# Kernel tuning notes

Measured on AMD Instinct MI355X. Metric: run time of the kernel, lower is better.

## Reference

```python
import jax, jax.numpy as jnp
import numpy as np

B = 16        # number of point clouds
NP = 4096     # points per cloud
RATIO = 0.25
RADIUS = 0.2
K = 64        # max_num_neighbors hardcoded in the torch module
S = int(NP * RATIO)  # sampled centers per cloud
C_IN = 64


def setup_inputs() -> dict:
    key = jax.random.key(0)
    ks = jax.random.split(key, 6)
    x = jax.random.normal(ks[0], (B * NP, C_IN), dtype=jnp.float32)
    pos = jax.random.uniform(ks[1], (B * NP, 3), dtype=jnp.float32)  # unit cube
    batch = jnp.repeat(jnp.arange(B, dtype=jnp.int64), NP)
    d0, d1, d2, d3 = C_IN + 3, 64, 64, 128  # local_nn dims
    W1 = jax.random.normal(ks[2], (d0, d1), dtype=jnp.float32) / np.sqrt(d0)
    W2 = jax.random.normal(ks[3], (d1, d2), dtype=jnp.float32) / np.sqrt(d1)
    W3 = jax.random.normal(ks[4], (d2, d3), dtype=jnp.float32) / np.sqrt(d2)
    b1 = jnp.zeros((d1,), jnp.float32)
    b2 = jnp.zeros((d2,), jnp.float32)
    b3 = jnp.zeros((d3,), jnp.float32)
    return {"x": x, "pos": pos, "batch": batch,
            "W1": W1, "b1": b1, "W2": W2, "b2": b2, "W3": W3, "b3": b3}


def _fps(pos_b):
    """Farthest point sampling for one cloud. pos_b: [NP,3] -> [S] int32 indices."""
    dmin = jnp.sum((pos_b - pos_b[0]) ** 2, axis=-1)  # start from point 0

    def step(dmin, _):
        idx = jnp.argmax(dmin).astype(jnp.int32)
        dmin = jnp.minimum(dmin, jnp.sum((pos_b - pos_b[idx]) ** 2, axis=-1))
        return dmin, idx

    _, idxs = jax.lax.scan(step, dmin, None, length=S - 1)
    return jnp.concatenate([jnp.zeros((1,), jnp.int32), idxs])


def reference(x, pos, batch, W1, b1, W2, b2, W3, b3):
    xb = x.reshape(B, NP, -1)
    pb = pos.reshape(B, NP, 3)

    def per_cloud(xb_, pb_):
        idxs = _fps(pb_)                      # [S]
        centers = pb_[idxs]                   # [S,3]
        # ball query: up to K nearest neighbors within RADIUS (center itself always in-range)
        d2 = jnp.sum((centers[:, None, :] - pb_[None, :, :]) ** 2, axis=-1)  # [S,NP]
        neg = jnp.where(d2 <= RADIUS * RADIUS, -d2, -jnp.inf)
        vals, nbr = jax.lax.top_k(neg, K)     # [S,K]
        valid = jnp.isfinite(vals)            # [S,K]
        # PointConv message: local_nn(concat(x_j, pos_j - pos_i)), max-aggregated
        xj = xb_[nbr]                         # [S,K,C]
        rel = pb_[nbr] - centers[:, None, :]  # [S,K,3]
        h = jnp.concatenate([xj, rel], axis=-1)
        h = jax.nn.relu(h @ W1 + b1)
        h = jax.nn.relu(h @ W2 + b2)
        h = h @ W3 + b3                       # [S,K,Cout]
        h = jnp.where(valid[..., None], h, -jnp.inf)
        return jnp.max(h, axis=1), centers    # [S,Cout], [S,3]

    out, centers = jax.vmap(per_cloud)(xb, pb)
    x_out = out.reshape(B * S, -1)
    pos_out = centers.reshape(B * S, 3)
    batch_out = jnp.repeat(jnp.arange(B, dtype=batch.dtype), S)
    return x_out, pos_out, batch_out
```

## Files before the change

kernel.cpp:

```cpp
#include <hip/hip_runtime.h>
#include <math.h>

#define NB   16
#define NPTS 4096
#define SS   1024
#define KK   64
#define CIN  64
#define TPB  512
#define NWORK 240
#define GRID (NB + NWORK)
#define WPREP_N 20480

typedef unsigned short ushort_t;
typedef float vf2 __attribute__((ext_vector_type(2)));
typedef unsigned long long vu2 __attribute__((ext_vector_type(2)));
typedef short bf8v __attribute__((ext_vector_type(8)));
typedef float f4v __attribute__((ext_vector_type(4)));

__device__ __forceinline__ float dist2(float ax, float ay, float az,
                                       float bx, float by, float bz) {
#pragma clang fp contract(off)
  float dx = ax - bx, dy = ay - by, dz = az - bz;
  float a = dx * dx, b = dy * dy, c = dz * dz;
  return (a + b) + c;
}

__device__ __forceinline__ vf2 dist2v(vf2 x, vf2 y, vf2 z,
                                      vf2 cx, vf2 cy, vf2 cz) {
#pragma clang fp contract(off)
  vf2 dx = x - cx, dy = y - cy, dz = z - cz;
  vf2 a = dx * dx, b = dy * dy, c = dz * dz;
  return (a + b) + c;
}

__device__ __forceinline__ ushort_t f2bf(float f) {
  unsigned u = __float_as_uint(f);
  return (ushort_t)((u + 0x7FFFu + ((u >> 16) & 1u)) >> 16);
}

#define DPPMAX(v, ctrl, rmask)                                                 \
  fmaxf((v), __int_as_float(__builtin_amdgcn_update_dpp(                       \
                 __float_as_int(v), __float_as_int(v), (ctrl), (rmask), 0xf,   \
                 false)))

__global__ __launch_bounds__(256) void wprep_kernel(
    const float* __restrict__ W1, const float* __restrict__ W2,
    const float* __restrict__ W3, ushort_t* __restrict__ wbuf) {
  int i = blockIdx.x * 256 + threadIdx.x;
  if (i >= WPREP_N) return;
  float v;
  if (i < 6656) {
    int n = i / 104, k = i - n * 104;
    v = (k < 67) ? W1[k * 64 + n] : 0.f;
  } else if (i < 11264) {
    int j = i - 6656;
    int n = j / 72, k = j - n * 72;
    v = (k < 64) ? W2[k * 64 + n] : 0.f;
  } else {
    int j = i - 11264;
    int n = j / 72, k = j - n * 72;
    v = (k < 64) ? W3[k * 128 + n] : 0.f;
  }
  wbuf[i] = f2bf(v);
}

struct FpsS {
  float px[NPTS], py[NPTS], pz[NPTS];
  unsigned long long swk[2][4];
};
struct WrkS {
  ushort_t feat[64][104];
  ushort_t h1[64][72];
  union {
    unsigned long long ckey[1024];
    ushort_t h2[64][72];
  } u;
  float red[4][128];
  int nbr_s[KK];
  float cctr[3];
  int scnt;
};

__global__ __launch_bounds__(TPB) void fused_kernel(
    const float* __restrict__ pos, const float* __restrict__ x,
    const ushort_t* __restrict__ wbuf,
    const float* __restrict__ b1, const float* __restrict__ b2,
    const float* __restrict__ b3,
    float* __restrict__ centers4, int* __restrict__ prog,
    float* __restrict__ out_x, float* __restrict__ out_pos,
    float* __restrict__ out_batch) {
  __shared__ __align__(16) union { FpsS f; WrkS w; } S;
  const int t = threadIdx.x;

  if (blockIdx.x < NB) {
    asm volatile("s_setprio 3");
    const int b = blockIdx.x;
    const float* p = pos + (size_t)b * NPTS * 3;

    for (int j = t; j < NPTS * 3; j += TPB) {
      float v = p[j];
      int pt = j / 3, ch = j - pt * 3;
      if (ch == 0) S.f.px[pt] = v;
      else if (ch == 1) S.f.py[pt] = v;
      else S.f.pz[pt] = v;
    }
    for (int j = t; j < SS; j += TPB) out_batch[b * SS + j] = (float)b;
    __syncthreads();

    if (t < 256) {
      const int base = t * 16;
      vf2 x2[8], y2[8], z2[8], dm2[8];
      const float c0x = S.f.px[0], c0y = S.f.py[0], c0z = S.f.pz[0];
      {
        vf2 cX = {c0x, c0x}, cY = {c0y, c0y}, cZ = {c0z, c0z};
#pragma unroll
        for (int u = 0; u < 8; ++u) {
          x2[u].x = S.f.px[base + 2 * u]; x2[u].y = S.f.px[base + 2 * u + 1];
          y2[u].x = S.f.py[base + 2 * u]; y2[u].y = S.f.py[base + 2 * u + 1];
          z2[u].x = S.f.pz[base + 2 * u]; z2[u].y = S.f.pz[base + 2 * u + 1];
          dm2[u] = dist2v(x2[u], y2[u], z2[u], cX, cY, cZ);
        }
      }
      const int lane = t & 63, wid = t >> 6;
      const float BIG = 1e9f;
      int parity = 0;
      for (int s = 1; s < SS; ++s) {
        vf2 m0 = __builtin_elementwise_max(dm2[0], dm2[1]);
        vf2 m1 = __builtin_elementwise_max(dm2[2], dm2[3]);
        vf2 m2 = __builtin_elementwise_max(dm2[4], dm2[5]);
        vf2 m3 = __builtin_elementwise_max(dm2[6], dm2[7]);
        vf2 mm = __builtin_elementwise_max(
            __builtin_elementwise_max(m0, m1), __builtin_elementwise_max(m2, m3));
        float bv = fmaxf(mm.x, mm.y);
        float wv = bv;
        wv = DPPMAX(wv, 0x111, 0xf);
        wv = DPPMAX(wv, 0x112, 0xf);
        wv = DPPMAX(wv, 0x114, 0xf);
        wv = DPPMAX(wv, 0x118, 0xf);
        wv = DPPMAX(wv, 0x142, 0xa);
        wv = DPPMAX(wv, 0x143, 0xc);
        const float gvw =
            __int_as_float(__builtin_amdgcn_readlane(__float_as_int(wv), 63));
        unsigned long long mk = __ballot(bv == gvw);
        int fl = __ffsll((long long)mk) - 1;
        vf2 fcnt = {0.f, 1.f};
        vf2 best = {BIG, BIG};
#pragma unroll
        for (int u = 0; u < 8; ++u) {
          vf2 sv;
          sv.x = (dm2[u].x == gvw) ? fcnt.x : BIG;
          sv.y = (dm2[u].y == gvw) ? fcnt.y : BIG;
          best = __builtin_elementwise_min(best, sv);
          fcnt += (vf2){2.f, 2.f};
        }
        const int li = (int)fminf(best.x, best.y);
        if (lane == fl) {
          int gi = base + li;
          S.f.swk[parity][wid] =
              ((unsigned long long)__float_as_uint(gvw) << 32) |
              (unsigned)(~(unsigned)gi);
        }
        __syncthreads();
        const vu2* sp = (const vu2*)(&S.f.swk[parity][0]);
        vu2 q0 = sp[0], q1 = sp[1];
        unsigned long long bk = q0.x;
        bk = (q0.y > bk) ? q0.y : bk;
        bk = (q1.x > bk) ? q1.x : bk;
        bk = (q1.y > bk) ? q1.y : bk;
        const int gi = (int)(~(unsigned)bk);
        const float cx = S.f.px[gi], cy = S.f.py[gi], cz = S.f.pz[gi];
        {
          vf2 cX = {cx, cx}, cY = {cy, cy}, cZ = {cz, cz};
#pragma unroll
          for (int u = 0; u < 8; ++u) {
            vf2 d2 = dist2v(x2[u], y2[u], z2[u], cX, cY, cZ);
            dm2[u] = __builtin_elementwise_min(dm2[u], d2);
          }
        }
        parity ^= 1;
      }
      return;
    } else if (t < 320) {
      if (t == 256) {
        int r = b * SS;
        float c0x = S.f.px[0], c0y = S.f.py[0], c0z = S.f.pz[0];
        __hip_atomic_store(&centers4[r * 4 + 0], c0x, __ATOMIC_RELAXED, __HIP_MEMORY_SCOPE_AGENT);
        __hip_atomic_store(&centers4[r * 4 + 1], c0y, __ATOMIC_RELAXED, __HIP_MEMORY_SCOPE_AGENT);
        __hip_atomic_store(&centers4[r * 4 + 2], c0z, __ATOMIC_RELAXED, __HIP_MEMORY_SCOPE_AGENT);
        out_pos[r * 3 + 0] = c0x; out_pos[r * 3 + 1] = c0y; out_pos[r * 3 + 2] = c0z;
      }
      int parity = 0;
      for (int s = 1; s < SS; ++s) {
        __syncthreads();
        if (t == 256) {
          if ((s & 1) == 0) {
            asm volatile("s_waitcnt vmcnt(6)" ::: "memory");
            __hip_atomic_store(&prog[b * 32], s - 1, __ATOMIC_RELAXED, __HIP_MEMORY_SCOPE_AGENT);
          }
          const vu2* sp = (const vu2*)(&S.f.swk[parity][0]);
          vu2 q0 = sp[0], q1 = sp[1];
          unsigned long long bk = q0.x;
          bk = (q0.y > bk) ? q0.y : bk;
          bk = (q1.x > bk) ? q1.x : bk;
          bk = (q1.y > bk) ? q1.y : bk;
          const int gi = (int)(~(unsigned)bk);
          const float cx = S.f.px[gi], cy = S.f.py[gi], cz = S.f.pz[gi];
          int r = b * SS + s;
          __hip_atomic_store(&centers4[r * 4 + 0], cx, __ATOMIC_RELAXED, __HIP_MEMORY_SCOPE_AGENT);
          __hip_atomic_store(&centers4[r * 4 + 1], cy, __ATOMIC_RELAXED, __HIP_MEMORY_SCOPE_AGENT);
          __hip_atomic_store(&centers4[r * 4 + 2], cz, __ATOMIC_RELAXED, __HIP_MEMORY_SCOPE_AGENT);
          out_pos[r * 3 + 0] = cx; out_pos[r * 3 + 1] = cy; out_pos[r * 3 + 2] = cz;
        }
        parity ^= 1;
      }
      if (t == 256) {
        asm volatile("s_waitcnt vmcnt(0)" ::: "memory");
        __hip_atomic_store(&prog[b * 32], SS, __ATOMIC_RELAXED, __HIP_MEMORY_SCOPE_AGENT);
      }
      return;
    } else {
      for (int s = 1; s < SS; ++s) __syncthreads();
      return;
    }
  }

  const int w = blockIdx.x - NB;
  const int wv = t >> 6, lane = t & 63, lr = lane & 15, quad = lane >> 4;
  const int mrow = (wv << 4) + lr;
  const int mout = (wv << 4) + (quad << 2);
  const float R2 = 0.04f;

  for (int i = t; i < 64 * 14; i += TPB) {
    int r = i / 14, cp = i - r * 14;
    *(unsigned*)&S.w.feat[r][68 + 2 * cp] = 0;
  }
  if (t < 64) S.w.feat[t][67] = 0;

  for (int j = w; j < NB * SS; j += NWORK) {
    const int s = j >> 4, b = j & 15;
    const int c = b * SS + s;
    if (t == 0) {
      while (__hip_atomic_load(&prog[b * 32], __ATOMIC_RELAXED,
                               __HIP_MEMORY_SCOPE_AGENT) <= s)
        __builtin_amdgcn_s_sleep(2);
      S.w.cctr[0] = __hip_atomic_load(&centers4[c * 4 + 0], __ATOMIC_RELAXED, __HIP_MEMORY_SCOPE_AGENT);
      S.w.cctr[1] = __hip_atomic_load(&centers4[c * 4 + 1], __ATOMIC_RELAXED, __HIP_MEMORY_SCOPE_AGENT);
      S.w.cctr[2] = __hip_atomic_load(&centers4[c * 4 + 2], __ATOMIC_RELAXED, __HIP_MEMORY_SCOPE_AGENT);
      S.w.scnt = 0;
    }
    __syncthreads();
    const float cx = S.w.cctr[0], cy = S.w.cctr[1], cz = S.w.cctr[2];
    const float* p = pos + (size_t)b * NPTS * 3;

#pragma unroll
    for (int ii = 0; ii < NPTS / TPB; ++ii) {
      const int i = t + ii * TPB;
      float ax = p[i * 3 + 0], ay = p[i * 3 + 1], az = p[i * 3 + 2];
      float d2 = dist2(cx, cy, cz, ax, ay, az);
      if (d2 <= R2) {
        int sl = atomicAdd(&S.w.scnt, 1);
        if (sl < 1024)
          S.w.u.ckey[sl] =
              ((unsigned long long)__float_as_uint(d2) << 32) | (unsigned)i;
      }
    }
    __syncthreads();
    const int nv = min(S.w.scnt, 1024);
    const int nvp = (nv + 15) & ~15;
    for (int q = nv + t; q < nvp; q += TPB) S.w.u.ckey[q] = ~0ULL;
    if (t < KK) S.w.nbr_s[t] = -1;
    __syncthreads();

    for (int sI = t; sI < nv; sI += TPB) {
      const unsigned long long k = S.w.u.ckey[sI];
      int r = 0;
      for (int q = 0; q < nvp; q += 16) {
        const vu2* cp = (const vu2*)&S.w.u.ckey[q];
        vu2 a0 = cp[0], a1 = cp[1], a2 = cp[2], a3 = cp[3];
        vu2 a4 = cp[4], a5 = cp[5], a6 = cp[6], a7 = cp[7];
        r += (a0.x < k) + (a0.y < k) + (a1.x < k) + (a1.y < k);
        r += (a2.x < k) + (a2.y < k) + (a3.x < k) + (a3.y < k);
        r += (a4.x < k) + (a4.y < k) + (a5.x < k) + (a5.y < k);
        r += (a6.x < k) + (a6.y < k) + (a7.x < k) + (a7.y < k);
      }
      if (r < KK) S.w.nbr_s[r] = (int)(k & 0xFFFFFFFFu);
    }
    __syncthreads();

    {
      const int c2 = t & 31;
#pragma unroll
      for (int kq = 0; kq < 4; ++kq) {
        const int k = (t >> 5) + kq * 16;
        const int li = S.w.nbr_s[k];
        const int li2 = (li < 0) ? 0 : li;
        const float* xp = x + ((size_t)(b * NPTS + li2)) * CIN + 2 * c2;
        float vx = xp[0], vy = xp[1];
        if (li < 0) { vx = 0.f; vy = 0.f; }
        unsigned pk = ((unsigned)f2bf(vy) << 16) | (unsigned)f2bf(vx);
        *(unsigned*)&S.w.feat[k][2 * c2] = pk;
      }
    }
    if (t < 64) {
      const int li = S.w.nbr_s[t];
      const int li2 = (li < 0) ? 0 : li;
      const float* pp = p + (size_t)li2 * 3;
      float rx = pp[0] - cx, ry = pp[1] - cy, rz = pp[2] - cz;
      if (li < 0) { rx = 0.f; ry = 0.f; rz = 0.f; }
      S.w.feat[t][64] = f2bf(rx); S.w.feat[t][65] = f2bf(ry);
      S.w.feat[t][66] = f2bf(rz);
    }
    __syncthreads();

    if (t < 256) {
      f4v acc[4] = {{0,0,0,0},{0,0,0,0},{0,0,0,0},{0,0,0,0}};
#pragma unroll
      for (int kb = 0; kb < 3; ++kb) {
        const int ko = kb * 32 + quad * 8;
        bf8v a = *(const bf8v*)&S.w.feat[mrow][ko];
#pragma unroll
        for (int nb = 0; nb < 4; ++nb) {
          bf8v bb = *(const bf8v*)&wbuf[(nb * 16 + lr) * 104 + ko];
          acc[nb] = __builtin_amdgcn_mfma_f32_16x16x32_bf16(a, bb, acc[nb], 0, 0, 0);
        }
      }
#pragma unroll
      for (int nb = 0; nb < 4; ++nb) {
        const int n = nb * 16 + lr;
        const float bias = b1[n];
#pragma unroll
        for (int r = 0; r < 4; ++r)
          S.w.h1[mout + r][n] = f2bf(fmaxf(acc[nb][r] + bias, 0.f));
      }
    }
    __syncthreads();

    if (t < 256) {
      f4v acc[4] = {{0,0,0,0},{0,0,0,0},{0,0,0,0},{0,0,0,0}};
#pragma unroll
      for (int kb = 0; kb < 2; ++kb) {
        const int ko = kb * 32 + quad * 8;
        bf8v a = *(const bf8v*)&S.w.h1[mrow][ko];
#pragma unroll
        for (int nb = 0; nb < 4; ++nb) {
          bf8v bb = *(const bf8v*)&wbuf[6656 + (nb * 16 + lr) * 72 + ko];
          acc[nb] = __builtin_amdgcn_mfma_f32_16x16x32_bf16(a, bb, acc[nb], 0, 0, 0);
        }
      }
#pragma unroll
      for (int nb = 0; nb < 4; ++nb) {
        const int n = nb * 16 + lr;
        const float bias = b2[n];
#pragma unroll
        for (int r = 0; r < 4; ++r)
          S.w.u.h2[mout + r][n] = f2bf(fmaxf(acc[nb][r] + bias, 0.f));
      }
    }
    __syncthreads();

    if (t < 256) {
      f4v acc[8] = {{0,0,0,0},{0,0,0,0},{0,0,0,0},{0,0,0,0},
                    {0,0,0,0},{0,0,0,0},{0,0,0,0},{0,0,0,0}};
#pragma unroll
      for (int kb = 0; kb < 2; ++kb) {
        const int ko = kb * 32 + quad * 8;
        bf8v a = *(const bf8v*)&S.w.u.h2[mrow][ko];
#pragma unroll
        for (int nb = 0; nb < 8; ++nb) {
          bf8v bb = *(const bf8v*)&wbuf[11264 + (nb * 16 + lr) * 72 + ko];
          acc[nb] = __builtin_amdgcn_mfma_f32_16x16x32_bf16(a, bb, acc[nb], 0, 0, 0);
        }
      }
      float vmax[8];
#pragma unroll
      for (int nb = 0; nb < 8; ++nb) vmax[nb] = -INFINITY;
#pragma unroll
      for (int r = 0; r < 4; ++r) {
        if (S.w.nbr_s[mout + r] >= 0) {
#pragma unroll
          for (int nb = 0; nb < 8; ++nb) vmax[nb] = fmaxf(vmax[nb], acc[nb][r]);
        }
      }
#pragma unroll
      for (int nb = 0; nb < 8; ++nb) {
        float v = vmax[nb];
        v = fmaxf(v, __shfl_xor(v, 16));
        v = fmaxf(v, __shfl_xor(v, 32));
        if (quad == 0) S.w.red[wv][nb * 16 + lr] = v;
      }
    }
    __syncthreads();

    if (t < 128) {
      float m = fmaxf(fmaxf(S.w.red[0][t], S.w.red[1][t]),
                      fmaxf(S.w.red[2][t], S.w.red[3][t]));
      out_x[(size_t)c * 128 + t] = m + b3[t];
    }
  }
}

extern "C" void kernel_launch(void* const* d_in, const int* in_sizes, int n_in,
                              void* d_out, int out_size, void* d_ws, size_t ws_size,
                              hipStream_t stream) {
  const float* x   = (const float*)d_in[0];
  const float* pos = (const float*)d_in[1];
  const float* W1 = (const float*)d_in[3];
  const float* b1 = (const float*)d_in[4];
  const float* W2 = (const float*)d_in[5];
  const float* b2 = (const float*)d_in[6];
  const float* W3 = (const float*)d_in[7];
  const float* b3 = (const float*)d_in[8];

  float* centers4 = (float*)d_ws;
  int* prog       = (int*)(centers4 + (size_t)NB * SS * 4);
  ushort_t* wbuf  = (ushort_t*)(prog + NB * 32);

  float* out_x     = (float*)d_out;
  float* out_pos   = out_x + (size_t)NB * SS * 128;
  float* out_batch = out_pos + (size_t)NB * SS * 3;

  wprep_kernel<<<(WPREP_N + 255) / 256, 256, 0, stream>>>(W1, W2, W3, wbuf);
  fused_kernel<<<GRID, TPB, 0, stream>>>(pos, x, wbuf, b1, b2, b3,
                                         centers4, prog,
                                         out_x, out_pos, out_batch);
}
```

Baseline: 824.2 us.

## Process two sampled centers per work iteration with wave-aggregated ball-query appends

Each worker block now handles a pair of consecutive centers from the same cloud. Positions are loaded once and tested against both centers, and the rank-sort is split across two halves of the block. All eight waves now run the MLP MFMA stages instead of four, and the reductions write two output rows. Per-thread shared-memory atomics are replaced with a ballot plus a single leader atomic per wave. The trade-offs are a lower candidate cap (768 instead of 1024), higher LDS use, and waiting for the later of the two FPS centers before starting.

```diff
diff --git a/kernel.cpp b/kernel.cpp
--- a/kernel.cpp
+++ b/kernel.cpp
@@ -10,6 +10,7 @@
 #define NWORK 240
 #define GRID (NB + NWORK)
 #define WPREP_N 20480
+#define BQCAP 768
 
 typedef unsigned short ushort_t;
 typedef float vf2 __attribute__((ext_vector_type(2)));
@@ -69,16 +70,16 @@
   unsigned long long swk[2][4];
 };
 struct WrkS {
-  ushort_t feat[64][104];
-  ushort_t h1[64][72];
+  ushort_t feat[128][104];
+  ushort_t h1[128][72];
   union {
-    unsigned long long ckey[1024];
-    ushort_t h2[64][72];
+    unsigned long long ckey[2 * BQCAP];
+    ushort_t h2[128][72];
   } u;
-  float red[4][128];
-  int nbr_s[KK];
-  float cctr[3];
-  int scnt;
+  float red[8][128];
+  int nbr_s[128];
+  float cctr[6];
+  int scnt[2];
 };
 
 __global__ __launch_bounds__(TPB) void fused_kernel(
@@ -230,67 +231,113 @@
   const int mout = (wv << 4) + (quad << 2);
   const float R2 = 0.04f;
 
-  for (int i = t; i < 64 * 14; i += TPB) {
+  for (int i = t; i < 128 * 14; i += TPB) {
     int r = i / 14, cp = i - r * 14;
     *(unsigned*)&S.w.feat[r][68 + 2 * cp] = 0;
   }
-  if (t < 64) S.w.feat[t][67] = 0;
-
-  for (int j = w; j < NB * SS; j += NWORK) {
-    const int s = j >> 4, b = j & 15;
-    const int c = b * SS + s;
+  if (t < 128) S.w.feat[t][67] = 0;
+
+  for (int j = w; j < NB * SS / 2; j += NWORK) {
+    const int sp = j >> 4, b = j & 15;
+    const int s1 = sp * 2 + 1;
+    const int c0 = b * SS + sp * 2, c1 = c0 + 1;
     if (t == 0) {
       while (__hip_atomic_load(&prog[b * 32], __ATOMIC_RELAXED,
-                               __HIP_MEMORY_SCOPE_AGENT) <= s)
+                               __HIP_MEMORY_SCOPE_AGENT) <= s1)
         __builtin_amdgcn_s_sleep(2);
-      S.w.cctr[0] = __hip_atomic_load(&centers4[c * 4 + 0], __ATOMIC_RELAXED, __HIP_MEMORY_SCOPE_AGENT);
-      S.w.cctr[1] = __hip_atomic_load(&centers4[c * 4 + 1], __ATOMIC_RELAXED, __HIP_MEMORY_SCOPE_AGENT);
-      S.w.cctr[2] = __hip_atomic_load(&centers4[c * 4 + 2], __ATOMIC_RELAXED, __HIP_MEMORY_SCOPE_AGENT);
-      S.w.scnt = 0;
-    }
-    __syncthreads();
-    const float cx = S.w.cctr[0], cy = S.w.cctr[1], cz = S.w.cctr[2];
+      S.w.cctr[0] = __hip_atomic_load(&centers4[c0 * 4 + 0], __ATOMIC_RELAXED, __HIP_MEMORY_SCOPE_AGENT);
+      S.w.cctr[1] = __hip_atomic_load(&centers4[c0 * 4 + 1], __ATOMIC_RELAXED, __HIP_MEMORY_SCOPE_AGENT);
+      S.w.cctr[2] = __hip_atomic_load(&centers4[c0 * 4 + 2], __ATOMIC_RELAXED, __HIP_MEMORY_SCOPE_AGENT);
+      S.w.cctr[3] = __hip_atomic_load(&centers4[c1 * 4 + 0], __ATOMIC_RELAXED, __HIP_MEMORY_SCOPE_AGENT);
+      S.w.cctr[4] = __hip_atomic_load(&centers4[c1 * 4 + 1], __ATOMIC_RELAXED, __HIP_MEMORY_SCOPE_AGENT);
+      S.w.cctr[5] = __hip_atomic_load(&centers4[c1 * 4 + 2], __ATOMIC_RELAXED, __HIP_MEMORY_SCOPE_AGENT);
+      S.w.scnt[0] = 0; S.w.scnt[1] = 0;
+    }
+    __syncthreads();
+    const float cax = S.w.cctr[0], cay = S.w.cctr[1], caz = S.w.cctr[2];
+    const float cbx = S.w.cctr[3], cby = S.w.cctr[4], cbz = S.w.cctr[5];
     const float* p = pos + (size_t)b * NPTS * 3;
 
 #pragma unroll
     for (int ii = 0; ii < NPTS / TPB; ++ii) {
       const int i = t + ii * TPB;
       float ax = p[i * 3 + 0], ay = p[i * 3 + 1], az = p[i * 3 + 2];
-      float d2 = dist2(cx, cy, cz, ax, ay, az);
-      if (d2 <= R2) {
-        int sl = atomicAdd(&S.w.scnt, 1);
-        if (sl < 1024)
-          S.w.u.ckey[sl] =
-              ((unsigned long long)__float_as_uint(d2) << 32) | (unsigned)i;
-      }
-    }
-    __syncthreads();
-    const int nv = min(S.w.scnt, 1024);
-    const int nvp = (nv + 15) & ~15;
-    for (int q = nv + t; q < nvp; q += TPB) S.w.u.ckey[q] = ~0ULL;
-    if (t < KK) S.w.nbr_s[t] = -1;
-    __syncthreads();
-
-    for (int sI = t; sI < nv; sI += TPB) {
-      const unsigned long long k = S.w.u.ckey[sI];
-      int r = 0;
-      for (int q = 0; q < nvp; q += 16) {
-        const vu2* cp = (const vu2*)&S.w.u.ckey[q];
-        vu2 a0 = cp[0], a1 = cp[1], a2 = cp[2], a3 = cp[3];
-        vu2 a4 = cp[4], a5 = cp[5], a6 = cp[6], a7 = cp[7];
-        r += (a0.x < k) + (a0.y < k) + (a1.x < k) + (a1.y < k);
-        r += (a2.x < k) + (a2.y < k) + (a3.x < k) + (a3.y < k);
-        r += (a4.x < k) + (a4.y < k) + (a5.x < k) + (a5.y < k);
-        r += (a6.x < k) + (a6.y < k) + (a7.x < k) + (a7.y < k);
-      }
-      if (r < KK) S.w.nbr_s[r] = (int)(k & 0xFFFFFFFFu);
+      float dA = dist2(cax, cay, caz, ax, ay, az);
+      float dB = dist2(cbx, cby, cbz, ax, ay, az);
+      bool hA = (dA <= R2), hB = (dB <= R2);
+      unsigned long long mA = __ballot(hA);
+      if (mA) {
+        int leader = __ffsll((long long)mA) - 1;
+        int base = 0;
+        if (lane == leader) base = atomicAdd(&S.w.scnt[0], __popcll(mA));
+        base = __shfl(base, leader, 64);
+        if (hA) {
+          int off = base + (int)__popcll(mA & ((1ULL << lane) - 1ULL));
+          if (off < BQCAP)
+            S.w.u.ckey[off] =
+                ((unsigned long long)__float_as_uint(dA) << 32) | (unsigned)i;
+        }
+      }
+      unsigned long long mB = __ballot(hB);
+      if (mB) {
+        int leader = __ffsll((long long)mB) - 1;
+        int base = 0;
+        if (lane == leader) base = atomicAdd(&S.w.scnt[1], __popcll(mB));
+        base = __shfl(base, leader, 64);
+        if (hB) {
+          int off = base + (int)__popcll(mB & ((1ULL << lane) - 1ULL));
+          if (off < BQCAP)
+            S.w.u.ckey[BQCAP + off] =
+                ((unsigned long long)__float_as_uint(dB) << 32) | (unsigned)i;
+        }
+      }
+    }
+    __syncthreads();
+    const int nvA = min(S.w.scnt[0], BQCAP), nvB = min(S.w.scnt[1], BQCAP);
+    const int nvpA = (nvA + 15) & ~15, nvpB = (nvB + 15) & ~15;
+    for (int q = nvA + t; q < nvpA; q += TPB) S.w.u.ckey[q] = ~0ULL;
+    for (int q = nvB + t; q < nvpB; q += TPB) S.w.u.ckey[BQCAP + q] = ~0ULL;
+    if (t < 128) S.w.nbr_s[t] = -1;
+    __syncthreads();
+
+    if (t < 256) {
+      for (int sI = t; sI < nvA; sI += 256) {
+        const unsigned long long k = S.w.u.ckey[sI];
+        int r = 0;
+        for (int q = 0; q < nvpA; q += 16) {
+          const vu2* cp = (const vu2*)&S.w.u.ckey[q];
+          vu2 a0 = cp[0], a1 = cp[1], a2 = cp[2], a3 = cp[3];
+          vu2 a4 = cp[4], a5 = cp[5], a6 = cp[6], a7 = cp[7];
+          r += (a0.x < k) + (a0.y < k) + (a1.x < k) + (a1.y < k);
+          r += (a2.x < k) + (a2.y < k) + (a3.x < k) + (a3.y < k);
+          r += (a4.x < k) + (a4.y < k) + (a5.x < k) + (a5.y < k);
+          r += (a6.x < k) + (a6.y < k) + (a7.x < k) + (a7.y < k);
+        }
+        if (r < KK) S.w.nbr_s[r] = (int)(k & 0xFFFFFFFFu);
+      }
+    } else {
+      const int t2 = t - 256;
+      for (int sI = t2; sI < nvB; sI += 256) {
+        const unsigned long long k = S.w.u.ckey[BQCAP + sI];
+        int r = 0;
+        for (int q = 0; q < nvpB; q += 16) {
+          const vu2* cp = (const vu2*)&S.w.u.ckey[BQCAP + q];
+          vu2 a0 = cp[0], a1 = cp[1], a2 = cp[2], a3 = cp[3];
+          vu2 a4 = cp[4], a5 = cp[5], a6 = cp[6], a7 = cp[7];
+          r += (a0.x < k) + (a0.y < k) + (a1.x < k) + (a1.y < k);
+          r += (a2.x < k) + (a2.y < k) + (a3.x < k) + (a3.y < k);
+          r += (a4.x < k) + (a4.y < k) + (a5.x < k) + (a5.y < k);
+          r += (a6.x < k) + (a6.y < k) + (a7.x < k) + (a7.y < k);
+        }
+        if (r < KK) S.w.nbr_s[64 + r] = (int)(k & 0xFFFFFFFFu);
+      }
     }
     __syncthreads();
 
     {
       const int c2 = t & 31;
 #pragma unroll
-      for (int kq = 0; kq < 4; ++kq) {
+      for (int kq = 0; kq < 8; ++kq) {
         const int k = (t >> 5) + kq * 16;
         const int li = S.w.nbr_s[k];
         const int li2 = (li < 0) ? 0 : li;
@@ -301,18 +348,21 @@
         *(unsigned*)&S.w.feat[k][2 * c2] = pk;
       }
     }
-    if (t < 64) {
+    if (t < 128) {
       const int li = S.w.nbr_s[t];
       const int li2 = (li < 0) ? 0 : li;
       const float* pp = p + (size_t)li2 * 3;
-      float rx = pp[0] - cx, ry = pp[1] - cy, rz = pp[2] - cz;
+      const float ccx = (t < 64) ? cax : cbx;
+      const float ccy = (t < 64) ? cay : cby;
+      const float ccz = (t < 64) ? caz : cbz;
+      float rx = pp[0] - ccx, ry = pp[1] - ccy, rz = pp[2] - ccz;
       if (li < 0) { rx = 0.f; ry = 0.f; rz = 0.f; }
       S.w.feat[t][64] = f2bf(rx); S.w.feat[t][65] = f2bf(ry);
       S.w.feat[t][66] = f2bf(rz);
     }
     __syncthreads();
 
-    if (t < 256) {
+    {
       f4v acc[4] = {{0,0,0,0},{0,0,0,0},{0,0,0,0},{0,0,0,0}};
 #pragma unroll
       for (int kb = 0; kb < 3; ++kb) {
@@ -335,7 +385,7 @@
     }
     __syncthreads();
 
-    if (t < 256) {
+    {
       f4v acc[4] = {{0,0,0,0},{0,0,0,0},{0,0,0,0},{0,0,0,0}};
 #pragma unroll
       for (int kb = 0; kb < 2; ++kb) {
@@ -358,7 +408,7 @@
     }
     __syncthreads();
 
-    if (t < 256) {
+    {
       f4v acc[8] = {{0,0,0,0},{0,0,0,0},{0,0,0,0},{0,0,0,0},
                     {0,0,0,0},{0,0,0,0},{0,0,0,0},{0,0,0,0}};
 #pragma unroll
@@ -394,7 +444,12 @@
     if (t < 128) {
       float m = fmaxf(fmaxf(S.w.red[0][t], S.w.red[1][t]),
                       fmaxf(S.w.red[2][t], S.w.red[3][t]));
-      out_x[(size_t)c * 128 + t] = m + b3[t];
+      out_x[(size_t)c0 * 128 + t] = m + b3[t];
+    } else if (t < 256) {
+      const int tt = t - 128;
+      float m = fmaxf(fmaxf(S.w.red[4][tt], S.w.red[5][tt]),
+                      fmaxf(S.w.red[6][tt], S.w.red[7][tt]));
+      out_x[(size_t)c1 * 128 + tt] = m + b3[tt];
     }
   }
 }
```

Result: faster. 752.5 us (-8.7%).
